# Kernel tuning notes

Hardware: AMD Instinct MI355X
Metric: run time of the kernel (lower is better)

Reference implementation:

```python
import jax, jax.numpy as jnp
import numpy as np

E = 64          # num_experts
D = 1024        # input_dim
BASE = 1024     # base_expert_units
K = 4           # k_top
B = 2048        # batch
EPS = 1e-5      # BatchNorm eps
SIZES = [int(BASE * (0.5 + i / (E - 1))) for i in range(E)]
SMAX = max(SIZES)  # 1536


def _cmask():
    m = np.zeros((E, SMAX), np.float32)
    for i, s in enumerate(SIZES):
        m[i, :s] = 1.0
    return jnp.asarray(m)


def setup_inputs() -> dict:
    key = jax.random.key(0)
    ks = jax.random.split(key, 16)
    cm = _cmask()  # [E, SMAX] valid-channel mask (pads zeroed)
    x = jax.random.normal(ks[0], (B, D), jnp.float32)
    W1 = jax.random.normal(ks[1], (E, D, SMAX), jnp.float32) * (1.0 / np.sqrt(D)) * cm[:, None, :]
    b1 = jax.random.normal(ks[2], (E, SMAX), jnp.float32) * 0.01 * cm
    g1 = jnp.ones((E, SMAX), jnp.float32) * cm            # BN1 gamma (0 in pad)
    be1 = jnp.zeros((E, SMAX), jnp.float32)               # BN1 beta
    m1 = jax.random.normal(ks[3], (E, SMAX), jnp.float32) * 0.01 * cm  # BN1 running mean
    v1 = (0.5 + jax.random.uniform(ks[4], (E, SMAX), jnp.float32)) * cm + (1.0 - cm)  # var=1 in pad
    W2 = jax.random.normal(ks[5], (E, SMAX, D), jnp.float32) * (1.0 / np.sqrt(SMAX)) * cm[:, :, None]
    b2 = jax.random.normal(ks[6], (E, D), jnp.float32) * 0.01
    g2 = jnp.ones((E, D), jnp.float32)
    be2 = jnp.zeros((E, D), jnp.float32)
    m2 = jax.random.normal(ks[7], (E, D), jnp.float32) * 0.01
    v2 = 0.5 + jax.random.uniform(ks[8], (E, D), jnp.float32)
    Wr = jax.random.normal(ks[9], (D, E), jnp.float32) * (1.0 / np.sqrt(D))
    br = jnp.zeros((E,), jnp.float32)
    return {"x": x, "W1": W1, "b1": b1, "g1": g1, "be1": be1, "m1": m1, "v1": v1,
            "W2": W2, "b2": b2, "g2": g2, "be2": be2, "m2": m2, "v2": v2,
            "Wr": Wr, "br": br}


def reference(x, W1, b1, g1, be1, m1, v1, W2, b2, g2, be2, m2, v2, Wr, br):
    # Router: top-k logits -> softmax over the k selected logits
    logits = x @ Wr + br                      # [B, E]
    topw, topi = jax.lax.top_k(logits, K)     # [B, K]
    topw = jax.nn.softmax(topw, axis=1)
    # Dense all-expert compute (padded-stacked; pads contribute exactly 0)
    h = jnp.einsum('bd,eds->ebs', x, W1) + b1[:, None, :]          # [E, B, SMAX]
    h = (h - m1[:, None, :]) * (g1 / jnp.sqrt(v1 + EPS))[:, None, :] + be1[:, None, :]
    h = jax.nn.relu(h)                        # Dropout is identity in eval
    y = jnp.einsum('ebs,esd->ebd', h, W2) + b2[:, None, :]         # [E, B, D]
    y = (y - m2[:, None, :]) * (g2 / jnp.sqrt(v2 + EPS))[:, None, :] + be2[:, None, :]
    eo = jnp.transpose(y, (1, 0, 2))          # [B, E, D]
    # Mask + detach of unselected experts (value-identical; affects grads only)
    mask = jax.nn.one_hot(topi, E, dtype=eo.dtype).sum(axis=1)[:, :, None]  # [B, E, 1]
    eo = eo * mask + jax.lax.stop_gradient(eo * (1.0 - mask))
    sel = jnp.take_along_axis(eo, topi[:, :, None], axis=1)        # [B, K, D]
    return jnp.sum(sel * topw[:, :, None], axis=1) + x
```

## Files before the change

### kernel.cpp

```cpp
#include <hip/hip_runtime.h>
#include <stdint.h>

#define E_    64
#define D_    1024
#define SMAX_ 1536
#define B_    2048
#define EPS_  1e-5f

typedef __attribute__((ext_vector_type(8))) __bf16 bf16x8;
typedef __attribute__((ext_vector_type(4))) float f32x4;

__device__ __forceinline__ unsigned int f2bf(float f) {
  unsigned int u = __float_as_uint(f);
  u += 0x7fffu + ((u >> 16) & 1u);
  return u >> 16;
}
__device__ __forceinline__ unsigned int f2bf_rn(float f) {
  return (__float_as_uint(f) + 0x8000u) >> 16;
}
__device__ __forceinline__ unsigned int pk2bf(float a, float b) {
  return __builtin_amdgcn_perm(__float_as_uint(b) + 0x8000u,
                               __float_as_uint(a) + 0x8000u, 0x07060302u);
}
__device__ __forceinline__ float bf2f(unsigned int s) {
  return __uint_as_float(s << 16);
}
__device__ __forceinline__ int expert_size(int e) {
  return (int)(1024.0 * (0.5 + (double)e / 63.0));
}

#define GLDS16(gp, lp) \
  __builtin_amdgcn_global_load_lds( \
      (const __attribute__((address_space(1))) unsigned int*)(const void*)(gp), \
      (__attribute__((address_space(3))) unsigned int*)(void*)(lp), 16, 0, 0)

__global__ void __launch_bounds__(256) router_kernel(
    const float* __restrict__ x, const float* __restrict__ Wr,
    const float* __restrict__ br, int* __restrict__ topi,
    float* __restrict__ topw, unsigned short* __restrict__ xbf)
{
  __shared__ float xs[D_];
  __shared__ double red[256];
  const int b = blockIdx.x, t = threadIdx.x;

  const float4* xr = (const float4*)(x + (size_t)b * D_);
  uint2* xbr = (uint2*)(xbf + (size_t)b * D_);
  for (int i = t; i < D_ / 4; i += 256) {
    float4 v = xr[i];
    xs[i * 4 + 0] = v.x; xs[i * 4 + 1] = v.y;
    xs[i * 4 + 2] = v.z; xs[i * 4 + 3] = v.w;
    uint2 p;
    p.x = pk2bf(v.x, v.y);
    p.y = pk2bf(v.z, v.w);
    xbr[i] = p;
  }
  __syncthreads();

  const int e = t & 63, q = t >> 6;
  const float* wp = Wr + (size_t)(q * 256) * E_ + e;
  double acc = 0.0;
#pragma unroll 8
  for (int d = 0; d < 256; d++)
    acc += (double)xs[q * 256 + d] * (double)wp[(size_t)d * E_];
  red[t] = acc;
  __syncthreads();

  if (t < 64) {
    double lg = red[t] + red[t + 64] + red[t + 128] + red[t + 192] + (double)br[t];
    double v = lg;
    double sel_v[4]; int sel_i[4];
#pragma unroll
    for (int k = 0; k < 4; k++) {
      double mv = v; int mi = t;
      for (int off = 32; off > 0; off >>= 1) {
        double ov = __shfl_down(mv, off);
        int    oi = __shfl_down(mi, off);
        if (ov > mv || (ov == mv && oi < mi)) { mv = ov; mi = oi; }
      }
      mv = __shfl(mv, 0); mi = __shfl(mi, 0);
      sel_v[k] = mv; sel_i[k] = mi;
      if (t == mi) v = -1e300;
    }
    if (t == 0) {
      double mx = sel_v[0], s = 0.0, w[4];
#pragma unroll
      for (int k = 0; k < 4; k++) { w[k] = exp(sel_v[k] - mx); s += w[k]; }
#pragma unroll
      for (int k = 0; k < 4; k++) {
        topi[b * 4 + k] = sel_i[k];
        topw[b * 4 + k] = (float)(w[k] / s);
      }
    }
  }
}

__global__ void __launch_bounds__(256) setup_kernel(
    const int* __restrict__ topi, const float* __restrict__ topw,
    int* __restrict__ counts, int* __restrict__ offs,
    int* __restrict__ tlist, float* __restrict__ wlist,
    int* __restrict__ slot_of)
{
  __shared__ int cnt[E_], base[E_], cur[E_];
  const int t = threadIdx.x;
  if (t < E_) cnt[t] = 0;
  __syncthreads();
  for (int i = t; i < B_ * 4; i += 256) atomicAdd(&cnt[topi[i]], 1);
  __syncthreads();
  if (t == 0) {
    int s = 0;
    for (int e = 0; e < E_; e++) { base[e] = s; s += cnt[e]; }
  }
  __syncthreads();
  if (t < E_) { counts[t] = cnt[t]; offs[t] = base[t]; cur[t] = 0; }
  __syncthreads();
  for (int i = t; i < B_ * 4; i += 256) {
    int e = topi[i];
    int p = atomicAdd(&cur[e], 1);
    int slot = base[e] + p;
    tlist[slot] = i >> 2;
    wlist[slot] = topw[i];
    slot_of[i] = slot;
  }
}

__global__ void __launch_bounds__(256, 2) gemm1_kernel(
    const unsigned short* __restrict__ xbf, const float* __restrict__ W1,
    const float* __restrict__ b1, const float* __restrict__ g1,
    const float* __restrict__ be1, const float* __restrict__ m1,
    const float* __restrict__ v1,
    const int* __restrict__ counts, const int* __restrict__ offs,
    const int* __restrict__ tlist, unsigned short* __restrict__ hbuf)
{
  const int e = blockIdx.x;
  const int s0 = blockIdx.y * 128;
  const int Se = expert_size(e);
  if (s0 >= Se) return;
  const int Ne = counts[e];
  if (Ne == 0) return;
  const int off = offs[e];

  __shared__ short lsA[192 * 32];
  __shared__ unsigned int lsB[128 * 17];
  __shared__ float lsAl[128], lsBt[128];

  const int t = threadIdx.x, lane = t & 63, wv = t >> 6;
  const int wm = wv >> 1, wn = wv & 1;

  if (t < 128) {
    int s = s0 + t;
    float al = g1[e * SMAX_ + s] * rsqrtf(v1[e * SMAX_ + s] + EPS_);
    lsAl[t] = al;
    lsBt[t] = (b1[e * SMAX_ + s] - m1[e * SMAX_ + s]) * al + be1[e * SMAX_ + s];
  }

  const int c = lane, j = wv;
  const float* Wb = W1 + (size_t)e * D_ * SMAX_ + s0 + 2 * c;
  unsigned int* wEven = lsB + (2 * c) * 17 + 4 * j;
  unsigned int* wOdd  = lsB + (2 * c + 1) * 17 + 4 * j;

  const int cs = (((lane & 3) ^ ((lane >> 2) & 3)) << 3);
  short* aDst0 = lsA + (wv * 48) * 32;
  short* aDst1 = lsA + (wv * 48 + 16) * 32;
  short* aDst2 = lsA + (wv * 48 + 32) * 32;

  const int aro = ((lane >> 4) ^ (lane & 3)) << 3;
  const int arow = wm * 96 + (lane & 15);
  const int nbase = wn * 64 + (lane & 15);
  const int bq = (lane >> 4) * 4;

  for (int m0 = 0; m0 < Ne; m0 += 192) {
    int row0 = m0 + wv * 48 + (lane >> 2);
    int sl0 = off + row0;          sl0 = sl0 < 8191 ? sl0 : 8191;
    int sl1 = off + row0 + 16;     sl1 = sl1 < 8191 ? sl1 : 8191;
    int sl2 = off + row0 + 32;     sl2 = sl2 < 8191 ? sl2 : 8191;
    const unsigned short* aSrc0 = xbf + (size_t)tlist[sl0] * D_ + cs;
    const unsigned short* aSrc1 = xbf + (size_t)tlist[sl1] * D_ + cs;
    const unsigned short* aSrc2 = xbf + (size_t)tlist[sl2] * D_ + cs;

    f32x4 acc[6][4] = {};
    float2 f[8];
#pragma unroll
    for (int i = 0; i < 8; i++)
      f[i] = *(const float2*)(Wb + (size_t)(j * 8 + i) * SMAX_);

    for (int k0 = 0; k0 < D_; k0 += 32) {
      __syncthreads();
      uint2 p0, p1;
      p0.x = pk2bf(f[0].x, f[1].x); p0.y = pk2bf(f[2].x, f[3].x);
      p1.x = pk2bf(f[4].x, f[5].x); p1.y = pk2bf(f[6].x, f[7].x);
      *(uint2*)(wEven)     = p0;
      *(uint2*)(wEven + 2) = p1;
      wOdd[0] = pk2bf(f[0].y, f[1].y);
      wOdd[1] = pk2bf(f[2].y, f[3].y);
      wOdd[2] = pk2bf(f[4].y, f[5].y);
      wOdd[3] = pk2bf(f[6].y, f[7].y);
      GLDS16(aSrc0 + k0, aDst0);
      GLDS16(aSrc1 + k0, aDst1);
      GLDS16(aSrc2 + k0, aDst2);
      __syncthreads();

      if (k0 + 32 < D_) {
#pragma unroll
        for (int i = 0; i < 8; i++)
          f[i] = *(const float2*)(Wb + (size_t)(k0 + 32 + j * 8 + i) * SMAX_);
      }

      bf16x8 af[6], bfr[4];
#pragma unroll
      for (int mt = 0; mt < 6; mt++)
        af[mt] = *(const bf16x8*)(lsA + (arow + mt * 16) * 32 + aro);
#pragma unroll
      for (int nt = 0; nt < 4; nt++) {
        int bb = (nbase + nt * 16) * 17 + bq;
        unsigned int r0 = lsB[bb], r1 = lsB[bb + 1], r2 = lsB[bb + 2], r3 = lsB[bb + 3];
        __attribute__((ext_vector_type(4))) unsigned int raw = {r0, r1, r2, r3};
        bfr[nt] = __builtin_bit_cast(bf16x8, raw);
      }
#pragma unroll
      for (int mt = 0; mt < 6; mt++)
#pragma unroll
        for (int nt = 0; nt < 4; nt++)
          acc[mt][nt] = __builtin_amdgcn_mfma_f32_16x16x32_bf16(af[mt], bfr[nt], acc[mt][nt], 0, 0, 0);
    }

#pragma unroll
    for (int mt = 0; mt < 6; mt++)
#pragma unroll
      for (int nt = 0; nt < 4; nt++) {
        int nc = wn * 64 + nt * 16 + (lane & 15);
        float al = lsAl[nc], bt = lsBt[nc];
#pragma unroll
        for (int r = 0; r < 4; r++) {
          int m = m0 + wm * 96 + mt * 16 + (lane >> 4) * 4 + r;
          if (m < Ne) {
            float v = acc[mt][nt][r] * al + bt;
            v = v > 0.f ? v : 0.f;
            hbuf[(size_t)(off + m) * SMAX_ + s0 + nc] = (unsigned short)f2bf_rn(v);
          }
        }
      }
  }
}

__global__ void __launch_bounds__(256, 2) gemm2_kernel(
    const unsigned short* __restrict__ hbuf, const float* __restrict__ W2,
    const float* __restrict__ b2, const float* __restrict__ g2,
    const float* __restrict__ be2, const float* __restrict__ m2,
    const float* __restrict__ v2,
    const int* __restrict__ counts, const int* __restrict__ offs,
    const float* __restrict__ wlist, unsigned short* __restrict__ ybuf)
{
  const int e = blockIdx.x;
  const int d0 = blockIdx.y * 128;
  const int Se = expert_size(e);
  const int Ne = counts[e];
  if (Ne == 0) return;
  const int off = offs[e];
  const int Kp = (Se + 31) & ~31;

  __shared__ short lsA[192 * 32];
  __shared__ unsigned int lsB[128 * 17];
  __shared__ float lsAl[128], lsBt[128];

  const int t = threadIdx.x, lane = t & 63, wv = t >> 6;
  const int wm = wv >> 1, wn = wv & 1;

  if (t < 128) {
    int d = d0 + t;
    float al = g2[e * D_ + d] * rsqrtf(v2[e * D_ + d] + EPS_);
    lsAl[t] = al;
    lsBt[t] = (b2[e * D_ + d] - m2[e * D_ + d]) * al + be2[e * D_ + d];
  }

  const int c = lane, j = wv;
  const float* Wb = W2 + (size_t)e * SMAX_ * D_ + d0 + 2 * c;
  unsigned int* wEven = lsB + (2 * c) * 17 + 4 * j;
  unsigned int* wOdd  = lsB + (2 * c + 1) * 17 + 4 * j;

  const int cs = (((lane & 3) ^ ((lane >> 2) & 3)) << 3);
  short* aDst0 = lsA + (wv * 48) * 32;
  short* aDst1 = lsA + (wv * 48 + 16) * 32;
  short* aDst2 = lsA + (wv * 48 + 32) * 32;

  const int aro = ((lane >> 4) ^ (lane & 3)) << 3;
  const int arow = wm * 96 + (lane & 15);
  const int nbase = wn * 64 + (lane & 15);
  const int bq = (lane >> 4) * 4;

  for (int m0 = 0; m0 < Ne; m0 += 192) {
    int row0 = m0 + wv * 48 + (lane >> 2);
    int sl0 = off + row0;          sl0 = sl0 < 8191 ? sl0 : 8191;
    int sl1 = off + row0 + 16;     sl1 = sl1 < 8191 ? sl1 : 8191;
    int sl2 = off + row0 + 32;     sl2 = sl2 < 8191 ? sl2 : 8191;
    const unsigned short* aSrc0 = hbuf + (size_t)sl0 * SMAX_ + cs;
    const unsigned short* aSrc1 = hbuf + (size_t)sl1 * SMAX_ + cs;
    const unsigned short* aSrc2 = hbuf + (size_t)sl2 * SMAX_ + cs;

    f32x4 acc[6][4] = {};
    float2 f[8];
#pragma unroll
    for (int i = 0; i < 8; i++)
      f[i] = *(const float2*)(Wb + (size_t)(j * 8 + i) * D_);

    for (int k0 = 0; k0 < Kp; k0 += 32) {
      __syncthreads();
      uint2 p0, p1;
      p0.x = pk2bf(f[0].x, f[1].x); p0.y = pk2bf(f[2].x, f[3].x);
      p1.x = pk2bf(f[4].x, f[5].x); p1.y = pk2bf(f[6].x, f[7].x);
      *(uint2*)(wEven)     = p0;
      *(uint2*)(wEven + 2) = p1;
      wOdd[0] = pk2bf(f[0].y, f[1].y);
      wOdd[1] = pk2bf(f[2].y, f[3].y);
      wOdd[2] = pk2bf(f[4].y, f[5].y);
      wOdd[3] = pk2bf(f[6].y, f[7].y);
      GLDS16(aSrc0 + k0, aDst0);
      GLDS16(aSrc1 + k0, aDst1);
      GLDS16(aSrc2 + k0, aDst2);
      __syncthreads();

      if (k0 + 32 < Kp) {
#pragma unroll
        for (int i = 0; i < 8; i++)
          f[i] = *(const float2*)(Wb + (size_t)(k0 + 32 + j * 8 + i) * D_);
      }

      bf16x8 af[6], bfr[4];
#pragma unroll
      for (int mt = 0; mt < 6; mt++)
        af[mt] = *(const bf16x8*)(lsA + (arow + mt * 16) * 32 + aro);
#pragma unroll
      for (int nt = 0; nt < 4; nt++) {
        int bb = (nbase + nt * 16) * 17 + bq;
        unsigned int r0 = lsB[bb], r1 = lsB[bb + 1], r2 = lsB[bb + 2], r3 = lsB[bb + 3];
        __attribute__((ext_vector_type(4))) unsigned int raw = {r0, r1, r2, r3};
        bfr[nt] = __builtin_bit_cast(bf16x8, raw);
      }
#pragma unroll
      for (int mt = 0; mt < 6; mt++)
#pragma unroll
        for (int nt = 0; nt < 4; nt++)
          acc[mt][nt] = __builtin_amdgcn_mfma_f32_16x16x32_bf16(af[mt], bfr[nt], acc[mt][nt], 0, 0, 0);
    }

#pragma unroll
    for (int mt = 0; mt < 6; mt++)
#pragma unroll
      for (int nt = 0; nt < 4; nt++) {
        int nc = wn * 64 + nt * 16 + (lane & 15);
        float al = lsAl[nc], bt = lsBt[nc];
#pragma unroll
        for (int r = 0; r < 4; r++) {
          int m = m0 + wm * 96 + mt * 16 + (lane >> 4) * 4 + r;
          if (m < Ne) {
            float wr = wlist[off + m];
            float v = acc[mt][nt][r] * al + bt;
            ybuf[(size_t)(off + m) * D_ + d0 + nc] = (unsigned short)f2bf_rn(wr * v);
          }
        }
      }
  }
}

__global__ void __launch_bounds__(256) gather_kernel(
    const float* __restrict__ x, const unsigned short* __restrict__ ybuf,
    const int* __restrict__ slot_of, float* __restrict__ out)
{
  const int b = blockIdx.x, t = threadIdx.x;
  int s[4];
#pragma unroll
  for (int k = 0; k < 4; k++) s[k] = slot_of[b * 4 + k];

  float4 xv = ((const float4*)(x + (size_t)b * D_))[t];
  float r0 = xv.x, r1 = xv.y, r2 = xv.z, r3 = xv.w;
#pragma unroll
  for (int k = 0; k < 4; k++) {
    uint2 p = ((const uint2*)(ybuf + (size_t)s[k] * D_))[t];
    r0 += bf2f(p.x & 0xffffu); r1 += bf2f(p.x >> 16);
    r2 += bf2f(p.y & 0xffffu); r3 += bf2f(p.y >> 16);
  }
  float4 o; o.x = r0; o.y = r1; o.z = r2; o.w = r3;
  ((float4*)(out + (size_t)b * D_))[t] = o;
}

extern "C" void kernel_launch(void* const* d_in, const int* in_sizes, int n_in,
                              void* d_out, int out_size, void* d_ws, size_t ws_size,
                              hipStream_t stream)
{
  const float* x   = (const float*)d_in[0];
  const float* W1  = (const float*)d_in[1];
  const float* b1  = (const float*)d_in[2];
  const float* g1  = (const float*)d_in[3];
  const float* be1 = (const float*)d_in[4];
  const float* m1  = (const float*)d_in[5];
  const float* v1  = (const float*)d_in[6];
  const float* W2  = (const float*)d_in[7];
  const float* b2  = (const float*)d_in[8];
  const float* g2  = (const float*)d_in[9];
  const float* be2 = (const float*)d_in[10];
  const float* m2  = (const float*)d_in[11];
  const float* v2  = (const float*)d_in[12];
  const float* Wr  = (const float*)d_in[13];
  const float* br  = (const float*)d_in[14];
  float* out = (float*)d_out;

  char* ws = (char*)d_ws;
  int*            topi    = (int*)(ws + 0);
  float*          topw    = (float*)(ws + 32768);
  int*            slot_of = (int*)(ws + 65536);
  int*            tlist   = (int*)(ws + 98304);
  float*          wlist   = (float*)(ws + 131072);
  int*            counts  = (int*)(ws + 163840);
  int*            offs    = (int*)(ws + 164096);
  unsigned short* xbf     = (unsigned short*)(ws + 196608);
  unsigned short* hbuf    = (unsigned short*)(ws + 4390912);
  unsigned short* ybuf    = (unsigned short*)(ws + 29556736);

  router_kernel<<<dim3(B_), dim3(256), 0, stream>>>(x, Wr, br, topi, topw, xbf);
  setup_kernel<<<dim3(1), dim3(256), 0, stream>>>(topi, topw, counts, offs, tlist, wlist, slot_of);
  gemm1_kernel<<<dim3(E_, 12), dim3(256), 0, stream>>>(xbf, W1, b1, g1, be1, m1, v1,
                                                       counts, offs, tlist, hbuf);
  gemm2_kernel<<<dim3(E_, 8), dim3(256), 0, stream>>>(hbuf, W2, b2, g2, be2, m2, v2,
                                                      counts, offs, wlist, ybuf);
  gather_kernel<<<dim3(B_), dim3(256), 0, stream>>>(x, ybuf, slot_of, out);
}
```

Before: 880.0 us.

## Double-buffer LDS tiles in expert GEMMs with explicit waitcnt pipelining

Both grouped expert GEMM kernels now keep two LDS buffers for the A (activations) and B (weights) tiles, with a two-deep register prefetch of fp32 weight strips. While one buffer is being consumed by MFMA, the other is packed and filled with async global-to-LDS loads. The fill is synchronised with explicit vmcnt/lgkmcnt waits and a single barrier per step instead of two __syncthreads. The goal is to overlap global latency with compute; the cost is double the LDS footprint, which may lower occupancy. gemm2 now pads K to a multiple of 64, and the setup kernel is widened to 1024 threads.

```diff
diff --git a/kernel.cpp b/kernel.cpp
--- a/kernel.cpp
+++ b/kernel.cpp
@@ -10,11 +10,6 @@
 typedef __attribute__((ext_vector_type(8))) __bf16 bf16x8;
 typedef __attribute__((ext_vector_type(4))) float f32x4;
 
-__device__ __forceinline__ unsigned int f2bf(float f) {
-  unsigned int u = __float_as_uint(f);
-  u += 0x7fffu + ((u >> 16) & 1u);
-  return u >> 16;
-}
 __device__ __forceinline__ unsigned int f2bf_rn(float f) {
   return (__float_as_uint(f) + 0x8000u) >> 16;
 }
@@ -33,6 +28,50 @@
   __builtin_amdgcn_global_load_lds( \
       (const __attribute__((address_space(1))) unsigned int*)(const void*)(gp), \
       (__attribute__((address_space(3))) unsigned int*)(void*)(lp), 16, 0, 0)
+
+#define PACKB(dE, dO, F) do { \
+  uint2 _p0, _p1; \
+  _p0.x = pk2bf(F[0].x, F[1].x); _p0.y = pk2bf(F[2].x, F[3].x); \
+  _p1.x = pk2bf(F[4].x, F[5].x); _p1.y = pk2bf(F[6].x, F[7].x); \
+  *(uint2*)(dE) = _p0; *(uint2*)((dE) + 2) = _p1; \
+  (dO)[0] = pk2bf(F[0].y, F[1].y); (dO)[1] = pk2bf(F[2].y, F[3].y); \
+  (dO)[2] = pk2bf(F[4].y, F[5].y); (dO)[3] = pk2bf(F[6].y, F[7].y); \
+} while (0)
+
+#define LOADF(F, strip, STRIDE) do { \
+  _Pragma("unroll") \
+  for (int _i = 0; _i < 8; _i++) \
+    F[_i] = *(const float2*)(Wb + (size_t)((strip) * 32 + j * 8 + _i) * (STRIDE)); \
+} while (0)
+
+#define STEP_COMPUTE(b) do { \
+  bf16x8 af[6], bfr[4]; \
+  _Pragma("unroll") \
+  for (int mt = 0; mt < 6; mt++) \
+    af[mt] = *(const bf16x8*)(&lsA[b][(arow + mt * 16) * 32 + aro]); \
+  _Pragma("unroll") \
+  for (int nt = 0; nt < 4; nt++) { \
+    int bb = (nbase + nt * 16) * 17 + bq; \
+    unsigned int r0 = lsB[b][bb], r1 = lsB[b][bb + 1]; \
+    unsigned int r2 = lsB[b][bb + 2], r3 = lsB[b][bb + 3]; \
+    __attribute__((ext_vector_type(4))) unsigned int raw = {r0, r1, r2, r3}; \
+    bfr[nt] = __builtin_bit_cast(bf16x8, raw); \
+  } \
+  asm volatile("s_waitcnt lgkmcnt(0)" ::: "memory"); \
+  __builtin_amdgcn_sched_barrier(0); \
+  _Pragma("unroll") \
+  for (int mt = 0; mt < 6; mt++) \
+    _Pragma("unroll") \
+    for (int nt = 0; nt < 4; nt++) \
+      acc[mt][nt] = __builtin_amdgcn_mfma_f32_16x16x32_bf16(af[mt], bfr[nt], acc[mt][nt], 0, 0, 0); \
+} while (0)
+
+#define STEP_SYNC(deep) do { \
+  if (deep) asm volatile("s_waitcnt vmcnt(8)" ::: "memory"); \
+  else      asm volatile("s_waitcnt vmcnt(0)" ::: "memory"); \
+  __builtin_amdgcn_sched_barrier(0); \
+  __builtin_amdgcn_s_barrier(); \
+} while (0)
 
 __global__ void __launch_bounds__(256) router_kernel(
     const float* __restrict__ x, const float* __restrict__ Wr,
@@ -94,7 +133,7 @@
   }
 }
 
-__global__ void __launch_bounds__(256) setup_kernel(
+__global__ void __launch_bounds__(1024) setup_kernel(
     const int* __restrict__ topi, const float* __restrict__ topw,
     int* __restrict__ counts, int* __restrict__ offs,
     int* __restrict__ tlist, float* __restrict__ wlist,
@@ -104,7 +143,7 @@
   const int t = threadIdx.x;
   if (t < E_) cnt[t] = 0;
   __syncthreads();
-  for (int i = t; i < B_ * 4; i += 256) atomicAdd(&cnt[topi[i]], 1);
+  for (int i = t; i < B_ * 4; i += 1024) atomicAdd(&cnt[topi[i]], 1);
   __syncthreads();
   if (t == 0) {
     int s = 0;
@@ -113,7 +152,7 @@
   __syncthreads();
   if (t < E_) { counts[t] = cnt[t]; offs[t] = base[t]; cur[t] = 0; }
   __syncthreads();
-  for (int i = t; i < B_ * 4; i += 256) {
+  for (int i = t; i < B_ * 4; i += 1024) {
     int e = topi[i];
     int p = atomicAdd(&cur[e], 1);
     int slot = base[e] + p;
@@ -139,8 +178,8 @@
   if (Ne == 0) return;
   const int off = offs[e];
 
-  __shared__ short lsA[192 * 32];
-  __shared__ unsigned int lsB[128 * 17];
+  __shared__ short lsA[2][192 * 32];
+  __shared__ unsigned int lsB[2][128 * 17];
   __shared__ float lsAl[128], lsBt[128];
 
   const int t = threadIdx.x, lane = t & 63, wv = t >> 6;
@@ -155,13 +194,18 @@
 
   const int c = lane, j = wv;
   const float* Wb = W1 + (size_t)e * D_ * SMAX_ + s0 + 2 * c;
-  unsigned int* wEven = lsB + (2 * c) * 17 + 4 * j;
-  unsigned int* wOdd  = lsB + (2 * c + 1) * 17 + 4 * j;
+  unsigned int* wE0 = &lsB[0][(2 * c) * 17 + 4 * j];
+  unsigned int* wO0 = &lsB[0][(2 * c + 1) * 17 + 4 * j];
+  unsigned int* wE1 = &lsB[1][(2 * c) * 17 + 4 * j];
+  unsigned int* wO1 = &lsB[1][(2 * c + 1) * 17 + 4 * j];
 
   const int cs = (((lane & 3) ^ ((lane >> 2) & 3)) << 3);
-  short* aDst0 = lsA + (wv * 48) * 32;
-  short* aDst1 = lsA + (wv * 48 + 16) * 32;
-  short* aDst2 = lsA + (wv * 48 + 32) * 32;
+  short* aD00 = &lsA[0][(wv * 48) * 32];
+  short* aD01 = &lsA[0][(wv * 48 + 16) * 32];
+  short* aD02 = &lsA[0][(wv * 48 + 32) * 32];
+  short* aD10 = &lsA[1][(wv * 48) * 32];
+  short* aD11 = &lsA[1][(wv * 48 + 16) * 32];
+  short* aD12 = &lsA[1][(wv * 48 + 32) * 32];
 
   const int aro = ((lane >> 4) ^ (lane & 3)) << 3;
   const int arow = wm * 96 + (lane & 15);
@@ -178,49 +222,38 @@
     const unsigned short* aSrc2 = xbf + (size_t)tlist[sl2] * D_ + cs;
 
     f32x4 acc[6][4] = {};
-    float2 f[8];
-#pragma unroll
-    for (int i = 0; i < 8; i++)
-      f[i] = *(const float2*)(Wb + (size_t)(j * 8 + i) * SMAX_);
-
-    for (int k0 = 0; k0 < D_; k0 += 32) {
-      __syncthreads();
-      uint2 p0, p1;
-      p0.x = pk2bf(f[0].x, f[1].x); p0.y = pk2bf(f[2].x, f[3].x);
-      p1.x = pk2bf(f[4].x, f[5].x); p1.y = pk2bf(f[6].x, f[7].x);
-      *(uint2*)(wEven)     = p0;
-      *(uint2*)(wEven + 2) = p1;
-      wOdd[0] = pk2bf(f[0].y, f[1].y);
-      wOdd[1] = pk2bf(f[2].y, f[3].y);
-      wOdd[2] = pk2bf(f[4].y, f[5].y);
-      wOdd[3] = pk2bf(f[6].y, f[7].y);
-      GLDS16(aSrc0 + k0, aDst0);
-      GLDS16(aSrc1 + k0, aDst1);
-      GLDS16(aSrc2 + k0, aDst2);
-      __syncthreads();
-
-      if (k0 + 32 < D_) {
-#pragma unroll
-        for (int i = 0; i < 8; i++)
-          f[i] = *(const float2*)(Wb + (size_t)(k0 + 32 + j * 8 + i) * SMAX_);
-      }
-
-      bf16x8 af[6], bfr[4];
-#pragma unroll
-      for (int mt = 0; mt < 6; mt++)
-        af[mt] = *(const bf16x8*)(lsA + (arow + mt * 16) * 32 + aro);
-#pragma unroll
-      for (int nt = 0; nt < 4; nt++) {
-        int bb = (nbase + nt * 16) * 17 + bq;
-        unsigned int r0 = lsB[bb], r1 = lsB[bb + 1], r2 = lsB[bb + 2], r3 = lsB[bb + 3];
-        __attribute__((ext_vector_type(4))) unsigned int raw = {r0, r1, r2, r3};
-        bfr[nt] = __builtin_bit_cast(bf16x8, raw);
-      }
-#pragma unroll
-      for (int mt = 0; mt < 6; mt++)
-#pragma unroll
-        for (int nt = 0; nt < 4; nt++)
-          acc[mt][nt] = __builtin_amdgcn_mfma_f32_16x16x32_bf16(af[mt], bfr[nt], acc[mt][nt], 0, 0, 0);
+    float2 fA[8], fB[8];
+
+    LOADF(fA, 0, SMAX_);
+    LOADF(fB, 1, SMAX_);
+    PACKB(wE0, wO0, fA);
+    GLDS16(aSrc0, aD00); GLDS16(aSrc1, aD01); GLDS16(aSrc2, aD02);
+    __builtin_amdgcn_sched_barrier(0);
+    LOADF(fA, 2, SMAX_);
+    asm volatile("s_waitcnt vmcnt(8)" ::: "memory");
+    asm volatile("s_waitcnt lgkmcnt(0)" ::: "memory");
+    __builtin_amdgcn_sched_barrier(0);
+    __builtin_amdgcn_s_barrier();
+
+    for (int x = 0; x < 32; x += 2) {
+      PACKB(wE1, wO1, fB);
+      GLDS16(aSrc0 + (x + 1) * 32, aD10);
+      GLDS16(aSrc1 + (x + 1) * 32, aD11);
+      GLDS16(aSrc2 + (x + 1) * 32, aD12);
+      __builtin_amdgcn_sched_barrier(0);
+      if (x + 3 < 32) LOADF(fB, x + 3, SMAX_);
+      STEP_COMPUTE(0);
+      STEP_SYNC(x + 3 < 32);
+      if (x + 2 < 32) {
+        PACKB(wE0, wO0, fA);
+        GLDS16(aSrc0 + (x + 2) * 32, aD00);
+        GLDS16(aSrc1 + (x + 2) * 32, aD01);
+        GLDS16(aSrc2 + (x + 2) * 32, aD02);
+        __builtin_amdgcn_sched_barrier(0);
+        if (x + 4 < 32) LOADF(fA, x + 4, SMAX_);
+      }
+      STEP_COMPUTE(1);
+      STEP_SYNC(x + 4 < 32);
     }
 
 #pragma unroll
@@ -256,10 +289,11 @@
   const int Ne = counts[e];
   if (Ne == 0) return;
   const int off = offs[e];
-  const int Kp = (Se + 31) & ~31;
-
-  __shared__ short lsA[192 * 32];
-  __shared__ unsigned int lsB[128 * 17];
+  const int Kp64 = (Se + 63) & ~63;
+  const int NSTEP = Kp64 >> 5;
+
+  __shared__ short lsA[2][192 * 32];
+  __shared__ unsigned int lsB[2][128 * 17];
   __shared__ float lsAl[128], lsBt[128];
 
   const int t = threadIdx.x, lane = t & 63, wv = t >> 6;
@@ -274,13 +308,18 @@
 
   const int c = lane, j = wv;
   const float* Wb = W2 + (size_t)e * SMAX_ * D_ + d0 + 2 * c;
-  unsigned int* wEven = lsB + (2 * c) * 17 + 4 * j;
-  unsigned int* wOdd  = lsB + (2 * c + 1) * 17 + 4 * j;
+  unsigned int* wE0 = &lsB[0][(2 * c) * 17 + 4 * j];
+  unsigned int* wO0 = &lsB[0][(2 * c + 1) * 17 + 4 * j];
+  unsigned int* wE1 = &lsB[1][(2 * c) * 17 + 4 * j];
+  unsigned int* wO1 = &lsB[1][(2 * c + 1) * 17 + 4 * j];
 
   const int cs = (((lane & 3) ^ ((lane >> 2) & 3)) << 3);
-  short* aDst0 = lsA + (wv * 48) * 32;
-  short* aDst1 = lsA + (wv * 48 + 16) * 32;
-  short* aDst2 = lsA + (wv * 48 + 32) * 32;
+  short* aD00 = &lsA[0][(wv * 48) * 32];
+  short* aD01 = &lsA[0][(wv * 48 + 16) * 32];
+  short* aD02 = &lsA[0][(wv * 48 + 32) * 32];
+  short* aD10 = &lsA[1][(wv * 48) * 32];
+  short* aD11 = &lsA[1][(wv * 48 + 16) * 32];
+  short* aD12 = &lsA[1][(wv * 48 + 32) * 32];
 
   const int aro = ((lane >> 4) ^ (lane & 3)) << 3;
   const int arow = wm * 96 + (lane & 15);
@@ -297,49 +336,38 @@
     const unsigned short* aSrc2 = hbuf + (size_t)sl2 * SMAX_ + cs;
 
     f32x4 acc[6][4] = {};
-    float2 f[8];
-#pragma unroll
-    for (int i = 0; i < 8; i++)
-      f[i] = *(const float2*)(Wb + (size_t)(j * 8 + i) * D_);
-
-    for (int k0 = 0; k0 < Kp; k0 += 32) {
-      __syncthreads();
-      uint2 p0, p1;
-      p0.x = pk2bf(f[0].x, f[1].x); p0.y = pk2bf(f[2].x, f[3].x);
-      p1.x = pk2bf(f[4].x, f[5].x); p1.y = pk2bf(f[6].x, f[7].x);
-      *(uint2*)(wEven)     = p0;
-      *(uint2*)(wEven + 2) = p1;
-      wOdd[0] = pk2bf(f[0].y, f[1].y);
-      wOdd[1] = pk2bf(f[2].y, f[3].y);
-      wOdd[2] = pk2bf(f[4].y, f[5].y);
-      wOdd[3] = pk2bf(f[6].y, f[7].y);
-      GLDS16(aSrc0 + k0, aDst0);
-      GLDS16(aSrc1 + k0, aDst1);
-      GLDS16(aSrc2 + k0, aDst2);
-      __syncthreads();
-
-      if (k0 + 32 < Kp) {
-#pragma unroll
-        for (int i = 0; i < 8; i++)
-          f[i] = *(const float2*)(Wb + (size_t)(k0 + 32 + j * 8 + i) * D_);
-      }
-
-      bf16x8 af[6], bfr[4];
-#pragma unroll
-      for (int mt = 0; mt < 6; mt++)
-        af[mt] = *(const bf16x8*)(lsA + (arow + mt * 16) * 32 + aro);
-#pragma unroll
-      for (int nt = 0; nt < 4; nt++) {
-        int bb = (nbase + nt * 16) * 17 + bq;
-        unsigned int r0 = lsB[bb], r1 = lsB[bb + 1], r2 = lsB[bb + 2], r3 = lsB[bb + 3];
-        __attribute__((ext_vector_type(4))) unsigned int raw = {r0, r1, r2, r3};
-        bfr[nt] = __builtin_bit_cast(bf16x8, raw);
-      }
-#pragma unroll
-      for (int mt = 0; mt < 6; mt++)
-#pragma unroll
-        for (int nt = 0; nt < 4; nt++)
-          acc[mt][nt] = __builtin_amdgcn_mfma_f32_16x16x32_bf16(af[mt], bfr[nt], acc[mt][nt], 0, 0, 0);
+    float2 fA[8], fB[8];
+
+    LOADF(fA, 0, D_);
+    LOADF(fB, 1, D_);
+    PACKB(wE0, wO0, fA);
+    GLDS16(aSrc0, aD00); GLDS16(aSrc1, aD01); GLDS16(aSrc2, aD02);
+    __builtin_amdgcn_sched_barrier(0);
+    LOADF(fA, 2, D_);
+    asm volatile("s_waitcnt vmcnt(8)" ::: "memory");
+    asm volatile("s_waitcnt lgkmcnt(0)" ::: "memory");
+    __builtin_amdgcn_sched_barrier(0);
+    __builtin_amdgcn_s_barrier();
+
+    for (int x = 0; x < NSTEP; x += 2) {
+      PACKB(wE1, wO1, fB);
+      GLDS16(aSrc0 + (x + 1) * 32, aD10);
+      GLDS16(aSrc1 + (x + 1) * 32, aD11);
+      GLDS16(aSrc2 + (x + 1) * 32, aD12);
+      __builtin_amdgcn_sched_barrier(0);
+      if (x + 3 < NSTEP) LOADF(fB, x + 3, D_);
+      STEP_COMPUTE(0);
+      STEP_SYNC(x + 3 < NSTEP);
+      if (x + 2 < NSTEP) {
+        PACKB(wE0, wO0, fA);
+        GLDS16(aSrc0 + (x + 2) * 32, aD00);
+        GLDS16(aSrc1 + (x + 2) * 32, aD01);
+        GLDS16(aSrc2 + (x + 2) * 32, aD02);
+        __builtin_amdgcn_sched_barrier(0);
+        if (x + 4 < NSTEP) LOADF(fA, x + 4, D_);
+      }
+      STEP_COMPUTE(1);
+      STEP_SYNC(x + 4 < NSTEP);
     }
 
 #pragma unroll
@@ -416,7 +444,7 @@
   unsigned short* ybuf    = (unsigned short*)(ws + 29556736);
 
   router_kernel<<<dim3(B_), dim3(256), 0, stream>>>(x, Wr, br, topi, topw, xbf);
-  setup_kernel<<<dim3(1), dim3(256), 0, stream>>>(topi, topw, counts, offs, tlist, wlist, slot_of);
+  setup_kernel<<<dim3(1), dim3(1024), 0, stream>>>(topi, topw, counts, offs, tlist, wlist, slot_of);
   gemm1_kernel<<<dim3(E_, 12), dim3(256), 0, stream>>>(xbf, W1, b1, g1, be1, m1, v1,
                                                        counts, offs, tlist, hbuf);
   gemm2_kernel<<<dim3(E_, 8), dim3(256), 0, stream>>>(hbuf, W2, b2, g2, be2, m2, v2,
```

After: 864.9 us. About the same (-1.7%).
